# Performance work log

Hardware: AMD Instinct MI355X
Metric: run time of the kernel (lower is better)

## Reference

```python
import jax, jax.numpy as jnp
import numpy as np

D_MODEL = 1024
NUM_HEADS = 16
ROPE_THETA = 10000.0


def _rope(v, pos, theta=ROPE_THETA):
    # v: [B, S, D] (full d_model, as in the original module), pos: [B, S] int
    d = v.shape[-1]
    inv_freq = theta ** (-jnp.arange(0, d, 2, dtype=jnp.float32) / d)  # [D/2]
    ang = pos.astype(jnp.float32)[..., None] * inv_freq  # [B, S, D/2]
    cos, sin = jnp.cos(ang), jnp.sin(ang)
    x1, x2 = v[..., ::2], v[..., 1::2]
    r1 = x1 * cos - x2 * sin
    r2 = x1 * sin + x2 * cos
    return jnp.stack([r1, r2], axis=-1).reshape(v.shape)


def setup_inputs() -> dict:
    key = jax.random.key(0)
    ks = jax.random.split(key, 6)
    B, S, D = 2, 2048, D_MODEL
    std = np.sqrt(2.0 / (D + D)).astype(np.float32)
    x = jax.random.normal(ks[0], (B, S, D), dtype=jnp.float32)
    token_positions = jnp.sort(jax.random.randint(ks[1], (B, S), 0, S), axis=-1).astype(jnp.int32)
    wq = jax.random.normal(ks[2], (D, D), dtype=jnp.float32) * std
    wk = jax.random.normal(ks[3], (D, D), dtype=jnp.float32) * std
    wv = jax.random.normal(ks[4], (D, D), dtype=jnp.float32) * std
    wo = jax.random.normal(ks[5], (D, D), dtype=jnp.float32) * std
    return {"x": x, "token_positions": token_positions, "wq": wq, "wk": wk, "wv": wv, "wo": wo}


def reference(x, token_positions, wq, wk, wv, wo):
    B, S, D = x.shape
    H = NUM_HEADS
    dk = D // H
    # Projections (nn.functional.linear: x @ W^T)
    q = x @ wq.T
    k = x @ wk.T
    v = x @ wv.T
    # In the original, Q/K are reshaped to heads and back before RoPE -> identity;
    # RoPE is applied over the FULL d_model dimension.
    q = _rope(q, token_positions)
    k = _rope(k, token_positions)
    # Split heads
    q = q.reshape(B, S, H, dk)
    k = k.reshape(B, S, H, dk)
    v = v.reshape(B, S, H, dk)
    scores = jnp.einsum('bqhd,bkhd->bhqk', q, k) / jnp.sqrt(jnp.asarray(dk, x.dtype))
    causal = jnp.tril(jnp.ones((S, S), dtype=bool))  # True where allowed
    scores = jnp.where(causal[None, None], scores, -jnp.inf)
    attn = jax.nn.softmax(scores, axis=-1)
    out = jnp.einsum('bhqk,bkhd->bqhd', attn, v).reshape(B, S, D)
    return out @ wo.T
```

## Files before the change

### kernel.cpp

```cpp
#include <hip/hip_runtime.h>
#include <hip/hip_bf16.h>
#include <math.h>

typedef __attribute__((ext_vector_type(8))) short bf16x8;
typedef __attribute__((ext_vector_type(4))) float f32x4;
typedef __attribute__((ext_vector_type(8))) float f32x8;

#define D_MODEL 1024
#define NHEADS  16
#define DK      64
#define BATCH   2
#define SEQ     2048

static __device__ __forceinline__ short f2bf(float f) {
    unsigned u = __builtin_bit_cast(unsigned, f);
    u = u + 0x7FFFu + ((u >> 16) & 1u);
    return (short)(u >> 16);
}
static __device__ __forceinline__ short f2bf_fast(float f) {
    return (short)((__builtin_bit_cast(unsigned, f) + 0x8000u) >> 16);
}
static __device__ __forceinline__ float bf2f(short s) {
    return __builtin_bit_cast(float, ((unsigned)(unsigned short)s) << 16);
}

typedef __attribute__((address_space(3))) unsigned int lds_uint;
typedef __attribute__((address_space(1))) const unsigned int glob_uint;
static __device__ __forceinline__ void gl2lds16(const short* g, short* l) {
    __builtin_amdgcn_global_load_lds((glob_uint*)g, (lds_uint*)l, 16, 0, 0);
}

__global__ void detect_kernel(const unsigned* __restrict__ x, int* __restrict__ flag)
{
    const int lane = threadIdx.x;
    const unsigned w = x[lane];
    const unsigned e = (w >> 7) & 0xFFu;
    const bool weird = (e >= 0x88u) || (e <= 0x5Fu);
    const unsigned long long m = __ballot(weird);
    if (lane == 0) *flag = (__popcll(m) >= 16) ? 1 : 0;
}

#define NX8 ((BATCH * SEQ * D_MODEL) / 8)
#define NW8 ((D_MODEL * D_MODEL) / 8)
__global__ void cvt_all_kernel(const void* __restrict__ x,  const void* __restrict__ wq,
                               const void* __restrict__ wk, const void* __restrict__ wv,
                               const void* __restrict__ wo,
                               __hip_bfloat16* __restrict__ xb,  __hip_bfloat16* __restrict__ wqb,
                               __hip_bfloat16* __restrict__ wkb, __hip_bfloat16* __restrict__ wvb,
                               __hip_bfloat16* __restrict__ wob,
                               const int* __restrict__ dtf)
{
    const int i = blockIdx.x * blockDim.x + threadIdx.x;
    if (i >= NX8 + 4 * NW8) return;
    const void* src; __hip_bfloat16* dst; int off;
    if (i < NX8) { src = x; dst = xb; off = i; }
    else {
        const int j = i - NX8, seg = j >> 17; off = j & (NW8 - 1);
        switch (seg) {
            case 0: src = wq; dst = wqb; break;
            case 1: src = wk; dst = wkb; break;
            case 2: src = wv; dst = wvb; break;
            default: src = wo; dst = wob; break;
        }
    }
    if (*dtf) {
        const f32x8 v = ((const f32x8*)src)[off];
        bf16x8 r;
#pragma unroll
        for (int j = 0; j < 8; ++j) r[j] = f2bf(v[j]);
        ((bf16x8*)dst)[off] = r;
    } else {
        ((bf16x8*)dst)[off] = ((const bf16x8*)src)[off];
    }
}

static __device__ __forceinline__ void gemm128_main(
    const short* __restrict__ A, const short* __restrict__ B,
    int K, int bm, int bn, f32x4 (&acc)[4][4], short* lds)
{
    const int tid  = threadIdx.x;
    const int lane = tid & 63;
    const int wave = tid >> 6;
    const int l16  = lane & 15;
    const int quad = lane >> 4;

    const int srow = lane >> 2;
    const int scg  = (lane & 3) ^ ((lane >> 3) & 3);
    const short* ag = A + (size_t)(bm + wave * 32 + srow) * K + scg * 8;
    const short* bg = B + (size_t)(bn + wave * 32 + srow) * K + scg * 8;
    const int dst = wave * 1024 + lane * 8;

    const int mrow = (wave >> 1) * 64;
    const int nrow = (wave & 1) * 64;
    const int ph   = ((quad ^ ((l16 >> 1) & 3))) * 8;

    auto stage = [&](int k0, int buf) {
        short* ad = lds + buf * 4096 + dst;
        short* bd = lds + 8192 + buf * 4096 + dst;
        gl2lds16(ag + k0, ad);
        gl2lds16(ag + k0 + (size_t)16 * K, ad + 512);
        gl2lds16(bg + k0, bd);
        gl2lds16(bg + k0 + (size_t)16 * K, bd + 512);
    };

    stage(0, 0);
    for (int k0 = 0, t = 0; k0 < K; k0 += 32, ++t) {
        __asm__ volatile("s_waitcnt vmcnt(0)" ::: "memory");
        __syncthreads();
        if (k0 + 32 < K) stage(k0 + 32, (t + 1) & 1);

        const short* Ab = lds + (t & 1) * 4096;
        const short* Bb = lds + 8192 + (t & 1) * 4096;
        bf16x8 a[4], b[4];
#pragma unroll
        for (int x = 0; x < 4; ++x)
            a[x] = *(const bf16x8*)(Ab + (mrow + x * 16 + l16) * 32 + ph);
#pragma unroll
        for (int y = 0; y < 4; ++y)
            b[y] = *(const bf16x8*)(Bb + (nrow + y * 16 + l16) * 32 + ph);
#pragma unroll
        for (int x = 0; x < 4; ++x)
#pragma unroll
            for (int y = 0; y < 4; ++y)
                acc[x][y] = __builtin_amdgcn_mfma_f32_16x16x32_bf16(
                    a[x], b[y], acc[x][y], 0, 0, 0);
    }
}

__global__ __launch_bounds__(256) void gemm_qkv_kernel(
    const __hip_bfloat16* __restrict__ xb,
    const __hip_bfloat16* __restrict__ wqb,
    const __hip_bfloat16* __restrict__ wkb,
    const __hip_bfloat16* __restrict__ wvb,
    __hip_bfloat16* __restrict__ Qb,
    __hip_bfloat16* __restrict__ Kb,
    __hip_bfloat16* __restrict__ Vt)
{
    __shared__ alignas(16) short lds[16384];
    const int wsel = blockIdx.x >> 3;
    const int bn   = (blockIdx.x & 7) * 128;
    const int bm   = blockIdx.y * 128;
    const short* W = (const short*)(wsel == 0 ? wqb : (wsel == 1 ? wkb : wvb));

    f32x4 acc[4][4];
#pragma unroll
    for (int x = 0; x < 4; ++x)
#pragma unroll
        for (int y = 0; y < 4; ++y) acc[x][y] = (f32x4){0.f, 0.f, 0.f, 0.f};

    gemm128_main((const short*)xb, W, D_MODEL, bm, bn, acc, lds);

    const int lane = threadIdx.x & 63;
    const int wave = threadIdx.x >> 6;
    const int l16  = lane & 15;
    const int quad = lane >> 4;
    __hip_bfloat16* Crm = (wsel == 1) ? Kb : Qb;

#pragma unroll
    for (int x = 0; x < 4; ++x)
#pragma unroll
        for (int y = 0; y < 4; ++y)
#pragma unroll
            for (int r = 0; r < 4; ++r) {
                const int row = bm + (wave >> 1) * 64 + x * 16 + quad * 4 + r;
                const int col = bn + (wave & 1) * 64 + y * 16 + l16;
                const __hip_bfloat16 v = __float2bfloat16(acc[x][y][r]);
                if (wsel == 2) {
                    const int hh = col >> 6, dcol = col & 63;
                    const int bb = row >> 11, ss = row & (SEQ - 1);
                    Vt[(((size_t)bb * NHEADS + hh) * DK + dcol) * SEQ + ss] = v;
                } else {
                    Crm[(size_t)row * D_MODEL + col] = v;
                }
            }
}

__global__ __launch_bounds__(256) void gemm_out_kernel(
    const __hip_bfloat16* __restrict__ AO,
    const __hip_bfloat16* __restrict__ wob,
    void* __restrict__ C, const int* __restrict__ dtf)
{
    __shared__ alignas(16) short lds[2][6144];
    const int tid  = threadIdx.x;
    const int lane = tid & 63;
    const int wave = tid >> 6;
    const int l16  = lane & 15;
    const int quad = lane >> 4;
    const int bn = blockIdx.x * 128;
    const int bm = blockIdx.y * 64;
    const bool c32 = (*dtf) != 0;
    const int K = D_MODEL;

    const int srow = lane >> 2;
    const int scg  = (lane & 3) ^ ((lane >> 3) & 3);
    const short* Ap = (const short*)AO;
    const short* Bp = (const short*)wob;
    const short* ag = Ap + (size_t)(bm + wave * 16 + srow) * K + scg * 8;
    const short* bg = Bp + (size_t)(bn + wave * 32 + srow) * K + scg * 8;

    const int nrow = wave * 32;
    const int ph   = ((quad ^ ((l16 >> 1) & 3))) * 8;

    f32x4 acc[4][2];
#pragma unroll
    for (int x = 0; x < 4; ++x)
#pragma unroll
        for (int y = 0; y < 2; ++y) acc[x][y] = (f32x4){0.f, 0.f, 0.f, 0.f};

    auto stage = [&](int k0, int buf) {
        gl2lds16(ag + k0, &lds[buf][wave * 512 + lane * 8]);
        gl2lds16(bg + k0, &lds[buf][2048 + wave * 1024 + lane * 8]);
        gl2lds16(bg + k0 + (size_t)16 * K, &lds[buf][2048 + wave * 1024 + 512 + lane * 8]);
    };

    stage(0, 0);
    for (int k0 = 0, t = 0; k0 < K; k0 += 32, ++t) {
        __asm__ volatile("s_waitcnt vmcnt(0)" ::: "memory");
        __syncthreads();
        if (k0 + 32 < K) stage(k0 + 32, (t + 1) & 1);

        const short* Ab = &lds[t & 1][0];
        const short* Bb = &lds[t & 1][2048];
        bf16x8 a[4], b[2];
#pragma unroll
        for (int x = 0; x < 4; ++x)
            a[x] = *(const bf16x8*)(Ab + (x * 16 + l16) * 32 + ph);
#pragma unroll
        for (int y = 0; y < 2; ++y)
            b[y] = *(const bf16x8*)(Bb + (nrow + y * 16 + l16) * 32 + ph);
#pragma unroll
        for (int x = 0; x < 4; ++x)
#pragma unroll
            for (int y = 0; y < 2; ++y)
                acc[x][y] = __builtin_amdgcn_mfma_f32_16x16x32_bf16(
                    a[x], b[y], acc[x][y], 0, 0, 0);
    }

#pragma unroll
    for (int x = 0; x < 4; ++x)
#pragma unroll
        for (int y = 0; y < 2; ++y)
#pragma unroll
            for (int r = 0; r < 4; ++r) {
                const int row = bm + x * 16 + quad * 4 + r;
                const int col = bn + nrow + y * 16 + l16;
                const size_t idx = (size_t)row * D_MODEL + col;
                if (c32) ((float*)C)[idx] = acc[x][y][r];
                else     ((__hip_bfloat16*)C)[idx] = __float2bfloat16(acc[x][y][r]);
            }
}

__global__ void rope_kernel(__hip_bfloat16* __restrict__ Q,
                            __hip_bfloat16* __restrict__ Kt,
                            const int* __restrict__ pos, int n8)
{
    const int idx = blockIdx.x * blockDim.x + threadIdx.x;
    if (idx >= n8) return;
    const int elem0 = idx * 8;
    const int bs = elem0 >> 10;
    const int i0 = (elem0 & (D_MODEL - 1)) >> 1;

    const float p = (float)pos[bs];
    bf16x8 q8 = *((bf16x8*)Q + idx);
    bf16x8 k8 = *((bf16x8*)Kt + idx);

#pragma unroll
    for (int j = 0; j < 4; ++j) {
        const float inv = exp2f((float)(i0 + j) * -0.02595256257f);
        const float ang = p * inv;
        const float c = cosf(ang), s = sinf(ang);
        const float q1 = bf2f(q8[2 * j]);
        const float q2 = bf2f(q8[2 * j + 1]);
        const float k1 = bf2f(k8[2 * j]);
        const float k2 = bf2f(k8[2 * j + 1]);
        q8[2 * j]     = f2bf(q1 * c - q2 * s);
        q8[2 * j + 1] = f2bf(q1 * s + q2 * c);
        k8[2 * j]     = f2bf(k1 * c - k2 * s);
        k8[2 * j + 1] = f2bf(k1 * s + k2 * c);
    }
    *((bf16x8*)Q + idx)  = q8;
    *((bf16x8*)Kt + idx) = k8;
}

__global__ __launch_bounds__(256) void flash_attn_kernel(
    __hip_bfloat16* QO,
    const __hip_bfloat16* __restrict__ Kt,
    const __hip_bfloat16* __restrict__ Vt)
{
    __shared__ alignas(16) short k_lds[2][64 * 64];
    __shared__ alignas(16) short v_lds[2][64 * 64];
    __shared__ alignas(16) short p_lds[4][16 * 64];

    const int lane = threadIdx.x & 63;
    const int wave = threadIdx.x >> 6;
    const int l16  = lane & 15;
    const int quad = lane >> 4;
    const int qt   = 31 - blockIdx.x;
    const int b    = blockIdx.y / NHEADS;
    const int h    = blockIdx.y % NHEADS;
    const size_t base  = (size_t)b * SEQ * D_MODEL + h * DK;
    const size_t vbase = (size_t)blockIdx.y * DK * SEQ;

    const short* Qp = (const short*)QO;
    const short* Kp = (const short*)Kt;
    const short* Vp = (const short*)Vt;

    const int q0 = qt * 64 + wave * 16;
    const bf16x8 aq0 = *(const bf16x8*)(Qp + base + (size_t)(q0 + l16) * D_MODEL + quad * 8);
    const bf16x8 aq1 = *(const bf16x8*)(Qp + base + (size_t)(q0 + l16) * D_MODEL + 32 + quad * 8);

    f32x4 o[4];
    float ls[4] = {0.f, 0.f, 0.f, 0.f};
#pragma unroll
    for (int g = 0; g < 4; ++g) o[g] = (f32x4){0.f, 0.f, 0.f, 0.f};

    const int srow = lane >> 3;
    const int scg  = (lane & 7) ^ srow;
    const short* kg = Kp + ((size_t)b * SEQ + wave * 16 + srow) * D_MODEL + h * DK + scg * 8;
    const short* vg = Vp + vbase + (size_t)(wave * 16 + srow) * SEQ + scg * 8;

    const int ph0 = (quad ^ (l16 & 7)) * 8;
    const int ph1 = ((4 + quad) ^ (l16 & 7)) * 8;

    auto stage = [&](int t, int buf) {
        const int kv0 = t * 64;
#pragma unroll
        for (int i = 0; i < 2; ++i)
            gl2lds16(kg + (size_t)(kv0 + i * 8) * D_MODEL,
                     k_lds[buf] + (wave * 16 + i * 8) * 64 + lane * 8);
#pragma unroll
        for (int i = 0; i < 2; ++i)
            gl2lds16(vg + (size_t)(i * 8) * SEQ + kv0,
                     v_lds[buf] + (wave * 16 + i * 8) * 64 + lane * 8);
    };

    auto process = [&](int buf, int kv0, bool masked) {
        const short* kb = k_lds[buf];
        f32x4 sfrag[4];
        __builtin_amdgcn_s_setprio(1);
#pragma unroll
        for (int g = 0; g < 4; ++g) {
            const int rowk = (g * 16 + l16) * 64;
            const bf16x8 bk0 = *(const bf16x8*)(kb + rowk + ph0);
            const bf16x8 bk1 = *(const bf16x8*)(kb + rowk + ph1);
            f32x4 c = (f32x4){0.f, 0.f, 0.f, 0.f};
            c = __builtin_amdgcn_mfma_f32_16x16x32_bf16(aq0, bk0, c, 0, 0, 0);
            c = __builtin_amdgcn_mfma_f32_16x16x32_bf16(aq1, bk1, c, 0, 0, 0);
            sfrag[g] = c;
        }
        __builtin_amdgcn_s_setprio(0);
#pragma unroll
        for (int r = 0; r < 4; ++r) {
            const int qrow = q0 + quad * 4 + r;
            const int prow = quad * 4 + r;
            float ps = 0.f;
#pragma unroll
            for (int g = 0; g < 4; ++g) {
                float p = __expf(sfrag[g][r] * 0.125f);
                if (masked && (kv0 + g * 16 + l16 > qrow)) p = 0.f;
                ps += p;
                p_lds[wave][prow * 64 +
                            (((2 * g + (l16 >> 3)) ^ (prow & 7)) << 3) + (l16 & 7)]
                    = f2bf_fast(p);
            }
            ls[r] += ps;
        }
        __asm__ volatile("s_waitcnt lgkmcnt(0)" ::: "memory");
        const bf16x8 ap0 = *(const bf16x8*)(&p_lds[wave][l16 * 64 + ph0]);
        const bf16x8 ap1 = *(const bf16x8*)(&p_lds[wave][l16 * 64 + ph1]);
        __builtin_amdgcn_s_setprio(1);
#pragma unroll
        for (int g = 0; g < 4; ++g) {
            const int rowv = (g * 16 + l16) * 64;
            const bf16x8 bv0 = *(const bf16x8*)(v_lds[buf] + rowv + ph0);
            const bf16x8 bv1 = *(const bf16x8*)(v_lds[buf] + rowv + ph1);
            o[g] = __builtin_amdgcn_mfma_f32_16x16x32_bf16(ap0, bv0, o[g], 0, 0, 0);
            o[g] = __builtin_amdgcn_mfma_f32_16x16x32_bf16(ap1, bv1, o[g], 0, 0, 0);
        }
        __builtin_amdgcn_s_setprio(0);
    };

    stage(0, 0);
    for (int t = 0; t <= qt; ++t) {
        __asm__ volatile("s_waitcnt vmcnt(0)" ::: "memory");
        __syncthreads();
        if (t < qt) stage(t + 1, (t + 1) & 1);
        process(t & 1, t * 64, t == qt);
    }

#pragma unroll
    for (int r = 0; r < 4; ++r) {
        float s = ls[r];
#pragma unroll
        for (int off = 1; off < 16; off <<= 1) s += __shfl_xor(s, off);
        ls[r] = s;
    }
#pragma unroll
    for (int g = 0; g < 4; ++g)
#pragma unroll
        for (int r = 0; r < 4; ++r) {
            const int row = q0 + quad * 4 + r;
            QO[base + (size_t)row * D_MODEL + g * 16 + l16] =
                __float2bfloat16(o[g][r] / fmaxf(ls[r], 1e-20f));
        }
}

extern "C" void kernel_launch(void* const* d_in, const int* in_sizes, int n_in,
                              void* d_out, int out_size, void* d_ws, size_t ws_size,
                              hipStream_t stream)
{
    (void)in_sizes; (void)n_in; (void)out_size; (void)ws_size;

    const void* x  = d_in[0];
    const int*  pos = (const int*)d_in[1];
    const void* wq = d_in[2];
    const void* wk = d_in[3];
    const void* wv = d_in[4];
    const void* wo = d_in[5];

    const int M = BATCH * SEQ;
    const int D = D_MODEL;
    const size_t MD = (size_t)M * D;
    const size_t DD = (size_t)D * D;

    int* dtf = (int*)d_ws;
    __hip_bfloat16* xb  = (__hip_bfloat16*)((char*)d_ws + 256);
    __hip_bfloat16* wqb = xb  + MD;
    __hip_bfloat16* wkb = wqb + DD;
    __hip_bfloat16* wvb = wkb + DD;
    __hip_bfloat16* wob = wvb + DD;
    __hip_bfloat16* Qb  = wob + DD;
    __hip_bfloat16* Vtb = Qb  + MD;
    __hip_bfloat16* Kb  = (__hip_bfloat16*)d_out;

    dim3 blk(256);

    hipLaunchKernelGGL(detect_kernel, dim3(1), dim3(64), 0, stream,
                       (const unsigned*)x, dtf);

    const int ncvt = NX8 + 4 * NW8;
    hipLaunchKernelGGL(cvt_all_kernel, dim3((ncvt + 255) / 256), blk, 0, stream,
                       x, wq, wk, wv, wo, xb, wqb, wkb, wvb, wob, dtf);

    hipLaunchKernelGGL(gemm_qkv_kernel, dim3(24, 32), blk, 0, stream,
                       xb, wqb, wkb, wvb, Qb, Kb, Vtb);

    const int nrope8 = (int)(MD / 8);
    hipLaunchKernelGGL(rope_kernel, dim3((nrope8 + 255) / 256), blk, 0, stream,
                       Qb, Kb, pos, nrope8);

    hipLaunchKernelGGL(flash_attn_kernel, dim3(SEQ / 64, BATCH * NHEADS), blk, 0, stream,
                       Qb, Kb, Vtb);

    hipLaunchKernelGGL(gemm_out_kernel, dim3(D / 128, M / 64), blk, 0, stream,
                       Qb, wob, d_out, dtf);
}
```

Measured before the change: 213.8 us.

## Split KV across waves in flash attention with register-resident P and LDS reduction

The flash attention kernel is restructured so each wave handles all 64 query rows against its own 32-row slice of a 128-wide KV tile, instead of 16 query rows against the full 64-wide tile. The S=K·Q^T layout lets P stay in registers as the MFMA A operand, which removes the P round-trip through LDS. Partial outputs and row sums are reduced across waves through LDS at the end. The 1/sqrt(dk) scale is folded into the RoPE kernel for Q, and the grid is reordered so heads vary fastest. In exchange it uses much more LDS (about 65KB), adds a final cross-wave reduction, and keeps a 64-entry output accumulator per thread, which raises register pressure. It also relies on the unnormalized softmax (no max subtraction) already used before.

```diff
diff --git a/kernel.cpp b/kernel.cpp
--- a/kernel.cpp
+++ b/kernel.cpp
@@ -3,6 +3,7 @@
 #include <math.h>
 
 typedef __attribute__((ext_vector_type(8))) short bf16x8;
+typedef __attribute__((ext_vector_type(4))) short short4x;
 typedef __attribute__((ext_vector_type(4))) float f32x4;
 typedef __attribute__((ext_vector_type(8))) float f32x8;
 
@@ -273,8 +274,8 @@
         const float q2 = bf2f(q8[2 * j + 1]);
         const float k1 = bf2f(k8[2 * j]);
         const float k2 = bf2f(k8[2 * j + 1]);
-        q8[2 * j]     = f2bf(q1 * c - q2 * s);
-        q8[2 * j + 1] = f2bf(q1 * s + q2 * c);
+        q8[2 * j]     = f2bf((q1 * c - q2 * s) * 0.125f);
+        q8[2 * j + 1] = f2bf((q1 * s + q2 * c) * 0.125f);
         k8[2 * j]     = f2bf(k1 * c - k2 * s);
         k8[2 * j + 1] = f2bf(k1 * s + k2 * c);
     }
@@ -282,127 +283,186 @@
     *((bf16x8*)Kt + idx) = k8;
 }
 
-__global__ __launch_bounds__(256) void flash_attn_kernel(
+__global__ __launch_bounds__(256, 2) void flash_attn_kernel(
     __hip_bfloat16* QO,
     const __hip_bfloat16* __restrict__ Kt,
     const __hip_bfloat16* __restrict__ Vt)
 {
-    __shared__ alignas(16) short k_lds[2][64 * 64];
-    __shared__ alignas(16) short v_lds[2][64 * 64];
-    __shared__ alignas(16) short p_lds[4][16 * 64];
+    __shared__ alignas(16) char pool[66560];
+    short* k_lds = (short*)pool;
+    short* v_lds = (short*)(pool + 32768);
 
     const int lane = threadIdx.x & 63;
     const int wave = threadIdx.x >> 6;
     const int l16  = lane & 15;
     const int quad = lane >> 4;
-    const int qt   = 31 - blockIdx.x;
-    const int b    = blockIdx.y / NHEADS;
-    const int h    = blockIdx.y % NHEADS;
+    const int qt   = 31 - blockIdx.y;
+    const int bh   = blockIdx.x;
+    const int b    = bh >> 4;
+    const int h    = bh & 15;
     const size_t base  = (size_t)b * SEQ * D_MODEL + h * DK;
-    const size_t vbase = (size_t)blockIdx.y * DK * SEQ;
+    const size_t vbase = (size_t)bh * DK * SEQ;
 
     const short* Qp = (const short*)QO;
     const short* Kp = (const short*)Kt;
     const short* Vp = (const short*)Vt;
 
-    const int q0 = qt * 64 + wave * 16;
-    const bf16x8 aq0 = *(const bf16x8*)(Qp + base + (size_t)(q0 + l16) * D_MODEL + quad * 8);
-    const bf16x8 aq1 = *(const bf16x8*)(Qp + base + (size_t)(q0 + l16) * D_MODEL + 32 + quad * 8);
-
-    f32x4 o[4];
+    bf16x8 aq[4][2];
+#pragma unroll
+    for (int qf = 0; qf < 4; ++qf)
+#pragma unroll
+        for (int ks = 0; ks < 2; ++ks)
+            aq[qf][ks] = *(const bf16x8*)(Qp + base +
+                (size_t)(qt * 64 + qf * 16 + l16) * D_MODEL + ks * 32 + quad * 8);
+
+    f32x4 o[4][4];
     float ls[4] = {0.f, 0.f, 0.f, 0.f};
 #pragma unroll
-    for (int g = 0; g < 4; ++g) o[g] = (f32x4){0.f, 0.f, 0.f, 0.f};
+    for (int qf = 0; qf < 4; ++qf)
+#pragma unroll
+        for (int nf = 0; nf < 4; ++nf) o[qf][nf] = (f32x4){0.f, 0.f, 0.f, 0.f};
 
     const int srow = lane >> 3;
     const int scg  = (lane & 7) ^ srow;
-    const short* kg = Kp + ((size_t)b * SEQ + wave * 16 + srow) * D_MODEL + h * DK + scg * 8;
-    const short* vg = Vp + vbase + (size_t)(wave * 16 + srow) * SEQ + scg * 8;
-
-    const int ph0 = (quad ^ (l16 & 7)) * 8;
-    const int ph1 = ((4 + quad) ^ (l16 & 7)) * 8;
+    const short* kg = Kp + ((size_t)b * SEQ + wave * 32 + srow) * D_MODEL + h * DK + scg * 8;
+    const int ge = (l16 & 8) | ((l16 & 7) ^ quad);
+    const int go = (l16 & 8) | ((l16 & 7) ^ (4 + quad));
+    const short* vgA = Vp + vbase + (size_t)(wave * 16 + quad) * SEQ + ge * 8;
+    const short* vgB = Vp + vbase + (size_t)(wave * 16 + 4 + quad) * SEQ + go * 8;
 
     auto stage = [&](int t, int buf) {
-        const int kv0 = t * 64;
-#pragma unroll
-        for (int i = 0; i < 2; ++i)
-            gl2lds16(kg + (size_t)(kv0 + i * 8) * D_MODEL,
-                     k_lds[buf] + (wave * 16 + i * 8) * 64 + lane * 8);
-#pragma unroll
-        for (int i = 0; i < 2; ++i)
-            gl2lds16(vg + (size_t)(i * 8) * SEQ + kv0,
-                     v_lds[buf] + (wave * 16 + i * 8) * 64 + lane * 8);
+        const int kv0 = t * 128;
+        short* kd = k_lds + buf * 8192 + (wave * 32) * 64 + lane * 8;
+#pragma unroll
+        for (int i = 0; i < 4; ++i)
+            gl2lds16(kg + (size_t)(kv0 + i * 8) * D_MODEL, kd + i * 8 * 64);
+        short* vd = v_lds + buf * 8192 + (wave * 16) * 128 + lane * 8;
+        gl2lds16(vgA + kv0,                 vd);
+        gl2lds16(vgB + kv0,                 vd + 4 * 128);
+        gl2lds16(vgA + (size_t)8 * SEQ + kv0, vd + 8 * 128);
+        gl2lds16(vgB + (size_t)8 * SEQ + kv0, vd + 12 * 128);
     };
 
-    auto process = [&](int buf, int kv0, bool masked) {
-        const short* kb = k_lds[buf];
-        f32x4 sfrag[4];
+    auto compute = [&](int buf, int kv0, bool last) {
+        const short* kb = k_lds + buf * 8192;
+        const short* vb = v_lds + buf * 8192;
+        bf16x8 ak[2][2];
+#pragma unroll
+        for (int kvf = 0; kvf < 2; ++kvf)
+#pragma unroll
+            for (int ks = 0; ks < 2; ++ks) {
+                const int row = wave * 32 + kvf * 16 + l16;
+                const int g = (ks * 4 + quad) ^ (l16 & 7);
+                ak[kvf][ks] = *(const bf16x8*)(kb + row * 64 + g * 8);
+            }
+        f32x4 s[2][4];
         __builtin_amdgcn_s_setprio(1);
 #pragma unroll
-        for (int g = 0; g < 4; ++g) {
-            const int rowk = (g * 16 + l16) * 64;
-            const bf16x8 bk0 = *(const bf16x8*)(kb + rowk + ph0);
-            const bf16x8 bk1 = *(const bf16x8*)(kb + rowk + ph1);
-            f32x4 c = (f32x4){0.f, 0.f, 0.f, 0.f};
-            c = __builtin_amdgcn_mfma_f32_16x16x32_bf16(aq0, bk0, c, 0, 0, 0);
-            c = __builtin_amdgcn_mfma_f32_16x16x32_bf16(aq1, bk1, c, 0, 0, 0);
-            sfrag[g] = c;
+        for (int kvf = 0; kvf < 2; ++kvf)
+#pragma unroll
+            for (int qf = 0; qf < 4; ++qf) {
+                f32x4 c = (f32x4){0.f, 0.f, 0.f, 0.f};
+                c = __builtin_amdgcn_mfma_f32_16x16x32_bf16(ak[kvf][0], aq[qf][0], c, 0, 0, 0);
+                c = __builtin_amdgcn_mfma_f32_16x16x32_bf16(ak[kvf][1], aq[qf][1], c, 0, 0, 0);
+                s[kvf][qf] = c;
+            }
+        __builtin_amdgcn_s_setprio(0);
+
+        bf16x8 pa[4];
+#pragma unroll
+        for (int qf = 0; qf < 4; ++qf) {
+            const int qrow = qt * 64 + qf * 16 + l16;
+#pragma unroll
+            for (int kvf = 0; kvf < 2; ++kvf)
+#pragma unroll
+                for (int r = 0; r < 4; ++r) {
+                    float p = __expf(s[kvf][qf][r]);
+                    if (last && (kv0 + wave * 32 + kvf * 16 + quad * 4 + r > qrow))
+                        p = 0.f;
+                    ls[qf] += p;
+                    pa[qf][kvf * 4 + r] = f2bf_fast(p);
+                }
         }
-        __builtin_amdgcn_s_setprio(0);
-#pragma unroll
-        for (int r = 0; r < 4; ++r) {
-            const int qrow = q0 + quad * 4 + r;
-            const int prow = quad * 4 + r;
-            float ps = 0.f;
-#pragma unroll
-            for (int g = 0; g < 4; ++g) {
-                float p = __expf(sfrag[g][r] * 0.125f);
-                if (masked && (kv0 + g * 16 + l16 > qrow)) p = 0.f;
-                ps += p;
-                p_lds[wave][prow * 64 +
-                            (((2 * g + (l16 >> 3)) ^ (prow & 7)) << 3) + (l16 & 7)]
-                    = f2bf_fast(p);
+
+        bf16x8 bv[4];
+#pragma unroll
+        for (int nf = 0; nf < 4; ++nf) {
+            const int d = nf * 16 + l16;
+#pragma unroll
+            for (int e = 0; e < 2; ++e) {
+                const int g  = wave * 4 + e * 2 + (quad >> 1);
+                const int gs = (g & 8) | ((g & 7) ^ (l16 & 7));
+                const short4x v4 = *(const short4x*)(vb + d * 128 + gs * 8 + (quad & 1) * 4);
+                bv[nf][e * 4 + 0] = v4[0];
+                bv[nf][e * 4 + 1] = v4[1];
+                bv[nf][e * 4 + 2] = v4[2];
+                bv[nf][e * 4 + 3] = v4[3];
             }
-            ls[r] += ps;
         }
-        __asm__ volatile("s_waitcnt lgkmcnt(0)" ::: "memory");
-        const bf16x8 ap0 = *(const bf16x8*)(&p_lds[wave][l16 * 64 + ph0]);
-        const bf16x8 ap1 = *(const bf16x8*)(&p_lds[wave][l16 * 64 + ph1]);
         __builtin_amdgcn_s_setprio(1);
 #pragma unroll
-        for (int g = 0; g < 4; ++g) {
-            const int rowv = (g * 16 + l16) * 64;
-            const bf16x8 bv0 = *(const bf16x8*)(v_lds[buf] + rowv + ph0);
-            const bf16x8 bv1 = *(const bf16x8*)(v_lds[buf] + rowv + ph1);
-            o[g] = __builtin_amdgcn_mfma_f32_16x16x32_bf16(ap0, bv0, o[g], 0, 0, 0);
-            o[g] = __builtin_amdgcn_mfma_f32_16x16x32_bf16(ap1, bv1, o[g], 0, 0, 0);
-        }
+        for (int qf = 0; qf < 4; ++qf)
+#pragma unroll
+            for (int nf = 0; nf < 4; ++nf)
+                o[qf][nf] = __builtin_amdgcn_mfma_f32_16x16x32_bf16(
+                    pa[qf], bv[nf], o[qf][nf], 0, 0, 0);
         __builtin_amdgcn_s_setprio(0);
     };
 
+    const int tmax = qt >> 1;
     stage(0, 0);
-    for (int t = 0; t <= qt; ++t) {
+    for (int t = 0; t < tmax; ++t) {
         __asm__ volatile("s_waitcnt vmcnt(0)" ::: "memory");
         __syncthreads();
-        if (t < qt) stage(t + 1, (t + 1) & 1);
-        process(t & 1, t * 64, t == qt);
-    }
-
-#pragma unroll
-    for (int r = 0; r < 4; ++r) {
-        float s = ls[r];
-#pragma unroll
-        for (int off = 1; off < 16; off <<= 1) s += __shfl_xor(s, off);
-        ls[r] = s;
-    }
-#pragma unroll
-    for (int g = 0; g < 4; ++g)
-#pragma unroll
-        for (int r = 0; r < 4; ++r) {
-            const int row = q0 + quad * 4 + r;
-            QO[base + (size_t)row * D_MODEL + g * 16 + l16] =
-                __float2bfloat16(o[g][r] / fmaxf(ls[r], 1e-20f));
-        }
+        stage(t + 1, (t + 1) & 1);
+        compute(t & 1, t * 128, false);
+    }
+    __asm__ volatile("s_waitcnt vmcnt(0)" ::: "memory");
+    __syncthreads();
+    if (tmax * 128 + wave * 32 <= qt * 64 + 63)
+        compute(tmax & 1, tmax * 128, true);
+
+#pragma unroll
+    for (int qf = 0; qf < 4; ++qf) {
+        ls[qf] += __shfl_xor(ls[qf], 16);
+        ls[qf] += __shfl_xor(ls[qf], 32);
+    }
+    __syncthreads();
+    float* red = (float*)pool;
+    float* lsb = (float*)(pool + 65536);
+#pragma unroll
+    for (int qf = 0; qf < 4; ++qf)
+#pragma unroll
+        for (int nf = 0; nf < 4; ++nf)
+            *(f32x4*)(red + ((wave * 16 + qf * 4 + nf) * 64 + lane) * 4) = o[qf][nf];
+    if (quad == 0)
+#pragma unroll
+        for (int qf = 0; qf < 4; ++qf) lsb[wave * 64 + qf * 16 + l16] = ls[qf];
+    __syncthreads();
+
+    f32x4 lden = (f32x4){0.f, 0.f, 0.f, 0.f};
+#pragma unroll
+    for (int w = 0; w < 4; ++w)
+        lden += *(const f32x4*)(lsb + w * 64 + wave * 16 + quad * 4);
+    f32x4 osum[4];
+#pragma unroll
+    for (int nf = 0; nf < 4; ++nf) {
+        f32x4 a = (f32x4){0.f, 0.f, 0.f, 0.f};
+#pragma unroll
+        for (int w = 0; w < 4; ++w)
+            a += *(const f32x4*)(red + ((w * 16 + wave * 4 + nf) * 64 + lane) * 4);
+        osum[nf] = a;
+    }
+    float inv[4];
+#pragma unroll
+    for (int r = 0; r < 4; ++r) inv[r] = 1.f / fmaxf(lden[r], 1e-20f);
+#pragma unroll
+    for (int nf = 0; nf < 4; ++nf)
+#pragma unroll
+        for (int r = 0; r < 4; ++r)
+            QO[base + (size_t)(qt * 64 + wave * 16 + quad * 4 + r) * D_MODEL
+                    + nf * 16 + l16]
+                = __float2bfloat16(osum[nf][r] * inv[r]);
 }
 
 extern "C" void kernel_launch(void* const* d_in, const int* in_sizes, int n_in,
@@ -449,7 +509,7 @@
     hipLaunchKernelGGL(rope_kernel, dim3((nrope8 + 255) / 256), blk, 0, stream,
                        Qb, Kb, pos, nrope8);
 
-    hipLaunchKernelGGL(flash_attn_kernel, dim3(SEQ / 64, BATCH * NHEADS), blk, 0, stream,
+    hipLaunchKernelGGL(flash_attn_kernel, dim3(32, 32), blk, 0, stream,
                        Qb, Kb, Vtb);
 
     hipLaunchKernelGGL(gemm_out_kernel, dim3(D / 128, M / 64), blk, 0, stream,
```

Result: faster. 186.1 us (-12.9%).
